# Kernel tuning notes

Measured on AMD Instinct MI355X. Metric: run time of the kernel, lower is better.

Reference implementation:

```python
import jax, jax.numpy as jnp
import numpy as np

DIM = 256
HEADS = 8
DIM_HEAD = 64
INNER = HEADS * DIM_HEAD  # 512
SCALE = DIM_HEAD ** -0.5
EPS = 1e-5


def _layernorm(x, w, b):
    mu = jnp.mean(x, axis=-1, keepdims=True)
    var = jnp.var(x, axis=-1, keepdims=True)
    return (x - mu) * jax.lax.rsqrt(var + EPS) * w + b


def setup_inputs() -> dict:
    key = jax.random.key(0)
    ks = jax.random.split(key, 20)
    B, N, M, H, W = 8, 4096, 256, 64, 64
    s = 0.02
    inp = {
        "feat": jax.random.normal(ks[0], (B, N, DIM), jnp.float32),
        "center": jax.random.normal(ks[1], (B, M, DIM), jnp.float32),
        "pos": jax.random.normal(ks[2], (B, DIM, H, W), jnp.float32),
        "center_pos": jax.random.normal(ks[3], (B, M, DIM), jnp.float32),
        # projection weights stored [in, out] so y = x @ W
        "Wq": jax.random.normal(ks[4], (DIM, INNER), jnp.float32) * s,
        "Wk": jax.random.normal(ks[5], (DIM, INNER), jnp.float32) * s,
        "Wv1": jax.random.normal(ks[6], (DIM, INNER), jnp.float32) * s,
        "Wv2": jax.random.normal(ks[7], (DIM, INNER), jnp.float32) * s,
        "Wo1": jax.random.normal(ks[8], (INNER, DIM), jnp.float32) * s,
        "Wo2": jax.random.normal(ks[9], (INNER, DIM), jnp.float32) * s,
        "ln1_w": jnp.ones((DIM,), jnp.float32),
        "ln1_b": jnp.zeros((DIM,), jnp.float32),
        "ln2_w": jnp.ones((DIM,), jnp.float32),
        "ln2_b": jnp.zeros((DIM,), jnp.float32),
        "ffn1_W1": jax.random.normal(ks[10], (DIM, DIM), jnp.float32) * s,
        "ffn1_W2": jax.random.normal(ks[11], (DIM, DIM), jnp.float32) * s,
        "ffn1_b2": jnp.zeros((DIM,), jnp.float32),
        "ffn2_W1": jax.random.normal(ks[12], (DIM, DIM), jnp.float32) * s,
        "ffn2_W2": jax.random.normal(ks[13], (DIM, DIM), jnp.float32) * s,
        "ffn2_b2": jnp.zeros((DIM,), jnp.float32),
    }
    return inp


def reference(feat, center, pos, center_pos, Wq, Wk, Wv1, Wv2, Wo1, Wo2,
              ln1_w, ln1_b, ln2_w, ln2_b, ffn1_W1, ffn1_W2, ffn1_b2,
              ffn2_W1, ffn2_W2, ffn2_b2):
    B = feat.shape[0]
    # pos: [B, C, H, W] -> [B, N, C]
    pos_f = pos.reshape(B, DIM, -1).transpose(0, 2, 1)
    q = (feat + pos_f) @ Wq            # [B, N, INNER]
    k = (center + center_pos) @ Wk     # [B, M, INNER]
    v1 = feat @ Wv1                    # [B, N, INNER]
    v2 = center @ Wv2                  # [B, M, INNER]

    def split(x):  # [B, T, h*d] -> [B, h, T, d]
        return x.reshape(B, x.shape[1], HEADS, DIM_HEAD).transpose(0, 2, 1, 3)

    q, k, v1, v2 = split(q), split(k), split(v1), split(v2)
    attn = jnp.einsum("bhnd,bhmd->bhnm", q, k) * SCALE  # [B, h, N, M]
    attn1 = jax.nn.softmax(attn, axis=-2)  # over N (queries)
    attn2 = jax.nn.softmax(attn, axis=-1)  # over M (keys)
    out_feat = jnp.einsum("bhnm,bhmd->bhnd", attn2, v2)    # [B, h, N, d]
    out_center = jnp.einsum("bhnm,bhnd->bhmd", attn1, v1)  # [B, h, M, d]

    def merge(x):  # [B, h, T, d] -> [B, T, h*d]
        return x.transpose(0, 2, 1, 3).reshape(B, x.shape[2], INNER)

    out_feat = merge(out_feat) @ Wo1 + feat
    out_center = merge(out_center) @ Wo2 + center
    out_feat = _layernorm(out_feat, ln1_w, ln1_b)
    out_center = _layernorm(out_center, ln2_w, ln2_b)
    out_feat = jax.nn.relu(out_feat @ ffn1_W1) @ ffn1_W2 + ffn1_b2 + out_feat
    out_center = jax.nn.relu(out_center @ ffn2_W1) @ ffn2_W2 + ffn2_b2 + out_center
    return out_feat, out_center
```

## Files before the change

### kernel.cpp

```cpp
#include <hip/hip_runtime.h>

typedef __bf16 bf16;
typedef __bf16 bf16x4 __attribute__((ext_vector_type(4)));
typedef __bf16 bf16x8 __attribute__((ext_vector_type(8)));
typedef float f32x4 __attribute__((ext_vector_type(4)));

#define MFMA16(a, b, c) __builtin_amdgcn_mfma_f32_16x16x32_bf16(a, b, c, 0, 0, 0)

#define CEXP 0.18033688011112042f

struct WTArgs {
  const float* src[10];
  bf16* dst[10];
  int K[10];
  int N[10];
};

__global__ __launch_bounds__(256) void wtrans_kernel(WTArgs args) {
  const int z = blockIdx.z;
  const int K = args.K[z], N = args.N[z];
  const int k0 = blockIdx.x * 64, n0 = blockIdx.y * 64;
  if (k0 >= K || n0 >= N) return;
  __shared__ float t[64][65];
  const int tx = threadIdx.x & 63, ty = threadIdx.x >> 6;
  const float* __restrict__ src = args.src[z];
  bf16* __restrict__ dst = args.dst[z];
#pragma unroll
  for (int i = 0; i < 16; ++i)
    t[ty + i * 4][tx] = src[(size_t)(k0 + ty + i * 4) * N + n0 + tx];
  __syncthreads();
#pragma unroll
  for (int i = 0; i < 16; ++i)
    dst[(size_t)(n0 + ty + i * 4) * K + k0 + tx] = (bf16)t[tx][ty + i * 4];
}

__global__ __launch_bounds__(256) void prep_xq_kernel(
    const float* __restrict__ feat, const float* __restrict__ pos,
    bf16* __restrict__ xq) {
  const int n0 = blockIdx.x * 64;
  const int c0 = blockIdx.y * 64;
  const int b = blockIdx.z;
  __shared__ float t[64][65];
  const int tx = threadIdx.x & 63, ty = threadIdx.x >> 6;
#pragma unroll
  for (int i = 0; i < 16; ++i) {
    int c = ty + i * 4;
    t[c][tx] = pos[((size_t)b * 256 + c0 + c) * 4096 + n0 + tx];
  }
  __syncthreads();
#pragma unroll
  for (int i = 0; i < 16; ++i) {
    int n = ty + i * 4;
    size_t off = ((size_t)b * 4096 + n0 + n) * 256 + c0 + tx;
    xq[off] = (bf16)(feat[off] + t[tx][n]);
  }
}

__global__ __launch_bounds__(256) void addvec_kernel(
    const float* __restrict__ a, const float* __restrict__ b,
    bf16* __restrict__ o, int n4) {
  int i = blockIdx.x * 256 + threadIdx.x;
  if (i < n4) {
    f32x4 x = ((const f32x4*)a)[i];
    f32x4 y = ((const f32x4*)b)[i];
    bf16x4 z;
#pragma unroll
    for (int j = 0; j < 4; ++j) z[j] = (bf16)(x[j] + y[j]);
    ((bf16x4*)o)[i] = z;
  }
}

template <typename TA>
__device__ inline bf16x8 ldA8(const TA* p);
template <>
__device__ inline bf16x8 ldA8<bf16>(const bf16* p) {
  return *(const bf16x8*)p;
}
template <>
__device__ inline bf16x8 ldA8<float>(const float* p) {
  f32x4 u = *(const f32x4*)p;
  f32x4 v = *((const f32x4*)p + 1);
  bf16x8 o;
#pragma unroll
  for (int i = 0; i < 4; ++i) {
    o[i] = (bf16)u[i];
    o[4 + i] = (bf16)v[i];
  }
  return o;
}

template <int EPI, typename TO, typename TR, typename TA>
__global__ __launch_bounds__(256) void gemm_kernel(
    const TA* __restrict__ A, const bf16* __restrict__ BT,
    TO* __restrict__ C, const TR* __restrict__ resid,
    const float* __restrict__ bias, int M, int N, int K) {
  const int m0 = blockIdx.x * 128;
  const int n0 = blockIdx.y * 128;
  const int tid = threadIdx.x;
  const int lane = tid & 63;
  const int w = tid >> 6;
  const int wr = (w >> 1) * 64, wc = (w & 1) * 64;
  const int l15 = lane & 15, quad = lane >> 4;

  __shared__ bf16 Al[128 * 40];
  __shared__ bf16 Bl[128 * 40];

  f32x4 acc[4][4];
#pragma unroll
  for (int i = 0; i < 4; ++i)
#pragma unroll
    for (int j = 0; j < 4; ++j) acc[i][j] = (f32x4){0.f, 0.f, 0.f, 0.f};

  for (int k0 = 0; k0 < K; k0 += 32) {
#pragma unroll
    for (int c = 0; c < 2; ++c) {
      int idx = tid + c * 256;
      int row = idx >> 2;
      int ko = (idx & 3) * 8;
      *(bf16x8*)(Al + row * 40 + ko) =
          ldA8(A + (size_t)(m0 + row) * K + k0 + ko);
      *(bf16x8*)(Bl + row * 40 + ko) =
          *(const bf16x8*)(BT + (size_t)(n0 + row) * K + k0 + ko);
    }
    __syncthreads();
    bf16x8 fa[4], fb[4];
#pragma unroll
    for (int i = 0; i < 4; ++i) {
      fa[i] = *(const bf16x8*)(Al + (wr + i * 16 + l15) * 40 + quad * 8);
      fb[i] = *(const bf16x8*)(Bl + (wc + i * 16 + l15) * 40 + quad * 8);
    }
#pragma unroll
    for (int i = 0; i < 4; ++i)
#pragma unroll
      for (int j = 0; j < 4; ++j)
        acc[i][j] = MFMA16(fa[i], fb[j], acc[i][j]);
    __syncthreads();
  }

#pragma unroll
  for (int i = 0; i < 4; ++i) {
#pragma unroll
    for (int r = 0; r < 4; ++r) {
      int row = m0 + wr + i * 16 + quad * 4 + r;
      size_t rb = (size_t)row * N + n0 + wc;
#pragma unroll
      for (int j = 0; j < 4; ++j) {
        int col = j * 16 + l15;
        float v = acc[i][j][r];
        if constexpr (EPI == 1) v = fmaxf(v, 0.f);
        if constexpr (EPI == 2) v += (float)resid[rb + col];
        if constexpr (EPI == 3)
          v += bias[n0 + wc + col] + (float)resid[rb + col];
        C[rb + col] = (TO)v;
      }
    }
  }
}

__global__ __launch_bounds__(256, 1) void attf_kernel(
    const bf16* q, const bf16* __restrict__ kk, const bf16* __restrict__ v1,
    const bf16* __restrict__ v2, bf16* af, float* __restrict__ acc_p,
    float* __restrict__ colsum_p) {
  const int nb = blockIdx.x;
  const int h = blockIdx.y;
  const int b = blockIdx.z;
  const int tid = threadIdx.x;
  const int lane = tid & 63;
  const int w = tid >> 6;
  const int l15 = lane & 15, quad = lane >> 4;

  __shared__ __align__(16) bf16 klds[256 * 72];
  __shared__ __align__(16) bf16 v2T[64 * 264];
  __shared__ __align__(16) bf16 v1T[2][64 * 72];
  __shared__ __align__(16) bf16 PT[256 * 72];
  __shared__ __align__(16) bf16 Pl[4][16 * 264];

#pragma unroll
  for (int c = 0; c < 8; ++c) {
    int idx = tid + c * 256;
    int m = idx >> 3;
    int dc = (idx & 7) * 8;
    *(bf16x8*)(klds + m * 72 + dc) =
        *(const bf16x8*)(kk + ((size_t)(b * 256 + m)) * 512 + h * 64 + dc);
  }
#pragma unroll
  for (int c = 0; c < 8; ++c) {
    int idx = tid + c * 256;
    int m = idx >> 3;
    int dc = (idx & 7) * 8;
    bf16x8 t =
        *(const bf16x8*)(v2 + ((size_t)(b * 256 + m)) * 512 + h * 64 + dc);
#pragma unroll
    for (int j = 0; j < 8; ++j) v2T[(dc + j) * 264 + m] = t[j];
  }
  {
    const int nl = tid >> 3;
    const int dc = (tid & 7) * 8;
    const bf16* v1b =
        v1 + ((size_t)(b * 4096 + nb * 1024)) * 512 + h * 64 + dc;
    bf16x8 t0 = *(const bf16x8*)(v1b + (size_t)nl * 512);
    bf16x8 t1 = *(const bf16x8*)(v1b + (size_t)(nl + 32) * 512);
#pragma unroll
    for (int j = 0; j < 8; ++j) {
      v1T[0][(dc + j) * 72 + nl] = t0[j];
      v1T[0][(dc + j) * 72 + nl + 32] = t1[j];
    }
  }
  bf16x8 qa0, qa1;
  {
    int nrow = b * 4096 + nb * 1024 + w * 16 + l15;
    const bf16* qp = q + (size_t)nrow * 512 + h * 64 + quad * 8;
    qa0 = *(const bf16x8*)(qp);
    qa1 = *(const bf16x8*)(qp + 32);
  }

  f32x4 oc2[16];
#pragma unroll
  for (int i = 0; i < 16; ++i) oc2[i] = (f32x4){0.f, 0.f, 0.f, 0.f};
  float cs[16];
#pragma unroll
  for (int i = 0; i < 16; ++i) cs[i] = 0.f;

  __syncthreads();

#pragma unroll 2
  for (int ch = 0; ch < 16; ++ch) {
    bf16x8 v1ra, v1rb;
    const int nl = tid >> 3;
    const int dc = (tid & 7) * 8;
    if (ch < 15) {
      const bf16* v1b =
          v1 + ((size_t)(b * 4096 + nb * 1024 + (ch + 1) * 64)) * 512 +
          h * 64 + dc;
      v1ra = *(const bf16x8*)(v1b + (size_t)nl * 512);
      v1rb = *(const bf16x8*)(v1b + (size_t)(nl + 32) * 512);
    }

    float rs[4] = {0.f, 0.f, 0.f, 0.f};
#pragma unroll
    for (int mt = 0; mt < 16; ++mt) {
      const bf16* kp = klds + (mt * 16 + l15) * 72 + quad * 8;
      bf16x8 b0 = *(const bf16x8*)(kp);
      bf16x8 b1 = *(const bf16x8*)(kp + 32);
      f32x4 s = (f32x4){0.f, 0.f, 0.f, 0.f};
      s = MFMA16(qa0, b0, s);
      s = MFMA16(qa1, b1, s);
      float e0 = exp2f(s[0] * CEXP);
      float e1 = exp2f(s[1] * CEXP);
      float e2 = exp2f(s[2] * CEXP);
      float e3 = exp2f(s[3] * CEXP);
      rs[0] += e0; rs[1] += e1; rs[2] += e2; rs[3] += e3;
      cs[mt] += e0 + e1 + e2 + e3;
      Pl[w][(quad * 4 + 0) * 264 + mt * 16 + l15] = (bf16)e0;
      Pl[w][(quad * 4 + 1) * 264 + mt * 16 + l15] = (bf16)e1;
      Pl[w][(quad * 4 + 2) * 264 + mt * 16 + l15] = (bf16)e2;
      Pl[w][(quad * 4 + 3) * 264 + mt * 16 + l15] = (bf16)e3;
      bf16x4 ev;
      ev[0] = (bf16)e0; ev[1] = (bf16)e1; ev[2] = (bf16)e2; ev[3] = (bf16)e3;
      *(bf16x4*)(PT + (mt * 16 + l15) * 72 + w * 16 + quad * 4) = ev;
    }
    if (ch < 15) {
      bf16* dst = v1T[(ch + 1) & 1];
#pragma unroll
      for (int j = 0; j < 8; ++j) {
        dst[(dc + j) * 72 + nl] = v1ra[j];
        dst[(dc + j) * 72 + nl + 32] = v1rb[j];
      }
    }
    __syncthreads();

    if (ch < 15) {
      int nrow = b * 4096 + nb * 1024 + (ch + 1) * 64 + w * 16 + l15;
      const bf16* qp = q + (size_t)nrow * 512 + h * 64 + quad * 8;
      qa0 = *(const bf16x8*)(qp);
      qa1 = *(const bf16x8*)(qp + 32);
    }

    f32x4 o1[4];
#pragma unroll
    for (int i = 0; i < 4; ++i) o1[i] = (f32x4){0.f, 0.f, 0.f, 0.f};
#pragma unroll
    for (int ks = 0; ks < 8; ++ks) {
      bf16x8 pa = *(const bf16x8*)(Pl[w] + l15 * 264 + ks * 32 + quad * 8);
#pragma unroll
      for (int dt = 0; dt < 4; ++dt) {
        bf16x8 vb = *(const bf16x8*)(v2T + (dt * 16 + l15) * 264 + ks * 32 +
                                     quad * 8);
        o1[dt] = MFMA16(pa, vb, o1[dt]);
      }
    }
    float inv[4];
#pragma unroll
    for (int r = 0; r < 4; ++r) {
      float v = rs[r];
      v += __shfl_xor(v, 1, 64);
      v += __shfl_xor(v, 2, 64);
      v += __shfl_xor(v, 4, 64);
      v += __shfl_xor(v, 8, 64);
      inv[r] = 1.f / v;
    }
#pragma unroll
    for (int dt = 0; dt < 4; ++dt) {
#pragma unroll
      for (int r = 0; r < 4; ++r) {
        int n = nb * 1024 + ch * 64 + w * 16 + quad * 4 + r;
        af[((size_t)(b * 4096 + n)) * 512 + h * 64 + dt * 16 + l15] =
            (bf16)(o1[dt][r] * inv[r]);
      }
    }

    const bf16* v1cur = v1T[ch & 1];
#pragma unroll
    for (int ks = 0; ks < 2; ++ks) {
      bf16x8 vb[4];
#pragma unroll
      for (int dt = 0; dt < 4; ++dt)
        vb[dt] = *(const bf16x8*)(v1cur + (dt * 16 + l15) * 72 + ks * 32 +
                                  quad * 8);
#pragma unroll
      for (int mq = 0; mq < 4; ++mq) {
        bf16x8 pa2 = *(const bf16x8*)(PT + (mq * 64 + w * 16 + l15) * 72 +
                                      ks * 32 + quad * 8);
#pragma unroll
        for (int dt = 0; dt < 4; ++dt)
          oc2[mq * 4 + dt] = MFMA16(pa2, vb[dt], oc2[mq * 4 + dt]);
      }
    }
    __syncthreads();
  }

  float* cw = (float*)klds;
#pragma unroll
  for (int t = 0; t < 16; ++t) {
    float v = cs[t];
    v += __shfl_xor(v, 16, 64);
    v += __shfl_xor(v, 32, 64);
    if (quad == 0) cw[w * 256 + t * 16 + l15] = v;
  }
  __syncthreads();
  {
    int m = tid;
    float s = cw[m] + cw[256 + m] + cw[512 + m] + cw[768 + m];
    colsum_p[((size_t)(nb * 64 + b * 8 + h)) * 256 + m] = s;
  }
  float* base = acc_p + ((size_t)(nb * 64 + b * 8 + h)) * 256 * 64;
#pragma unroll
  for (int mq = 0; mq < 4; ++mq) {
#pragma unroll
    for (int dt = 0; dt < 4; ++dt) {
#pragma unroll
      for (int r = 0; r < 4; ++r) {
        int m = mq * 64 + w * 16 + quad * 4 + r;
        base[m * 64 + dt * 16 + l15] = oc2[mq * 4 + dt][r];
      }
    }
  }
}

__global__ __launch_bounds__(256) void acm_kernel(
    const float* __restrict__ acc_p, const float* __restrict__ colsum_p,
    bf16* __restrict__ acm) {
  int idx = blockIdx.x * 256 + threadIdx.x;
  int d = idx & 63;
  int h = (idx >> 6) & 7;
  int m = (idx >> 9) & 255;
  int b = idx >> 17;
  float cv = 0.f, v = 0.f;
#pragma unroll
  for (int p = 0; p < 4; ++p) {
    cv += colsum_p[((size_t)(p * 64 + b * 8 + h)) * 256 + m];
    v += acc_p[(((size_t)(p * 64 + b * 8 + h)) * 256 + m) * 64 + d];
  }
  acm[idx] = (bf16)(v / cv);
}

__global__ __launch_bounds__(256) void ln_kernel(
    const bf16* __restrict__ x, const float* __restrict__ wv,
    const float* __restrict__ bv, bf16* __restrict__ y, int rows) {
  int wave = threadIdx.x >> 6;
  int lane = threadIdx.x & 63;
  int row = blockIdx.x * 4 + wave;
  if (row >= rows) return;
  const bf16* xr = x + (size_t)row * 256;
  bf16x4 v = *(const bf16x4*)(xr + lane * 4);
  float f0 = v[0], f1 = v[1], f2 = v[2], f3 = v[3];
  float s = f0 + f1 + f2 + f3;
  float ss = f0 * f0 + f1 * f1 + f2 * f2 + f3 * f3;
#pragma unroll
  for (int m = 1; m < 64; m <<= 1) {
    s += __shfl_xor(s, m, 64);
    ss += __shfl_xor(ss, m, 64);
  }
  float mean = s * (1.f / 256.f);
  float var = ss * (1.f / 256.f) - mean * mean;
  float rstd = rsqrtf(var + 1e-5f);
  f32x4 wq = *(const f32x4*)(wv + lane * 4);
  f32x4 bq = *(const f32x4*)(bv + lane * 4);
  bf16x4 o;
  o[0] = (bf16)((f0 - mean) * rstd * wq[0] + bq[0]);
  o[1] = (bf16)((f1 - mean) * rstd * wq[1] + bq[1]);
  o[2] = (bf16)((f2 - mean) * rstd * wq[2] + bq[2]);
  o[3] = (bf16)((f3 - mean) * rstd * wq[3] + bq[3]);
  *(bf16x4*)(y + (size_t)row * 256 + lane * 4) = o;
}

extern "C" void kernel_launch(void* const* d_in, const int* in_sizes, int n_in,
                              void* d_out, int out_size, void* d_ws,
                              size_t ws_size, hipStream_t stream) {
  const float* feat = (const float*)d_in[0];
  const float* center = (const float*)d_in[1];
  const float* pos = (const float*)d_in[2];
  const float* cpos = (const float*)d_in[3];
  const float* Wq = (const float*)d_in[4];
  const float* Wk = (const float*)d_in[5];
  const float* Wv1 = (const float*)d_in[6];
  const float* Wv2 = (const float*)d_in[7];
  const float* Wo1 = (const float*)d_in[8];
  const float* Wo2 = (const float*)d_in[9];
  const float* ln1w = (const float*)d_in[10];
  const float* ln1b = (const float*)d_in[11];
  const float* ln2w = (const float*)d_in[12];
  const float* ln2b = (const float*)d_in[13];
  const float* f1W1 = (const float*)d_in[14];
  const float* f1W2 = (const float*)d_in[15];
  const float* f1b2 = (const float*)d_in[16];
  const float* f2W1 = (const float*)d_in[17];
  const float* f2W2 = (const float*)d_in[18];
  const float* f2b2 = (const float*)d_in[19];

  char* ws = (char*)d_ws;
  const size_t MB = 1024 * 1024;
  bf16* q_ = (bf16*)(ws + 0);
  bf16* af_ = q_;
  bf16* v1_ = (bf16*)(ws + 32 * MB);
  bf16* xq_ = (bf16*)(ws + 64 * MB);
  float* accp_ = (float*)(ws + 64 * MB);
  bf16* rf_ = xq_;
  bf16* k_ = (bf16*)(ws + 80 * MB);
  bf16* xk_ = (bf16*)(ws + 82 * MB);
  bf16* rc_ = xk_;
  bf16* v2_ = (bf16*)(ws + 83 * MB);
  bf16* acm_ = v2_;
  float* colsum_ = (float*)(ws + 89 * MB);
  bf16* wt_ = (bf16*)(ws + 89 * MB + 262144);
  bf16* yf_ = q_;
  bf16* tf_ = (bf16*)(ws + 16 * MB);
  bf16* yc_ = (bf16*)(ws + 92 * MB);
  bf16* tc_ = (bf16*)(ws + 93 * MB);

  bf16* WqT = wt_;
  bf16* WkT = WqT + 131072;
  bf16* Wv1T = WkT + 131072;
  bf16* Wv2T = Wv1T + 131072;
  bf16* Wo1T = Wv2T + 131072;
  bf16* Wo2T = Wo1T + 131072;
  bf16* f1W1T = Wo2T + 131072;
  bf16* f1W2T = f1W1T + 65536;
  bf16* f2W1T = f1W2T + 65536;
  bf16* f2W2T = f2W1T + 65536;

  float* out_feat = (float*)d_out;
  float* out_center = out_feat + (size_t)8 * 4096 * 256;

  WTArgs wa;
  const float* srcs[10] = {Wq, Wk, Wv1, Wv2, Wo1, Wo2, f1W1, f1W2, f2W1, f2W2};
  bf16* dsts[10] = {WqT, WkT, Wv1T, Wv2T, Wo1T, Wo2T, f1W1T, f1W2T, f2W1T, f2W2T};
  int Ks[10] = {256, 256, 256, 256, 512, 512, 256, 256, 256, 256};
  int Ns[10] = {512, 512, 512, 512, 256, 256, 256, 256, 256, 256};
  for (int i = 0; i < 10; ++i) {
    wa.src[i] = srcs[i];
    wa.dst[i] = dsts[i];
    wa.K[i] = Ks[i];
    wa.N[i] = Ns[i];
  }

  wtrans_kernel<<<dim3(8, 8, 10), 256, 0, stream>>>(wa);
  prep_xq_kernel<<<dim3(64, 4, 8), 256, 0, stream>>>(feat, pos, xq_);
  addvec_kernel<<<dim3(512), 256, 0, stream>>>(center, cpos, xk_, 131072);

  gemm_kernel<0, bf16, bf16, bf16><<<dim3(256, 4), 256, 0, stream>>>(
      xq_, WqT, q_, nullptr, nullptr, 32768, 512, 256);
  gemm_kernel<0, bf16, bf16, bf16><<<dim3(16, 4), 256, 0, stream>>>(
      xk_, WkT, k_, nullptr, nullptr, 2048, 512, 256);
  gemm_kernel<0, bf16, bf16, float><<<dim3(256, 4), 256, 0, stream>>>(
      feat, Wv1T, v1_, nullptr, nullptr, 32768, 512, 256);
  gemm_kernel<0, bf16, bf16, float><<<dim3(16, 4), 256, 0, stream>>>(
      center, Wv2T, v2_, nullptr, nullptr, 2048, 512, 256);

  attf_kernel<<<dim3(4, 8, 8), 256, 0, stream>>>(q_, k_, v1_, v2_, af_, accp_,
                                                 colsum_);
  acm_kernel<<<dim3(4096), 256, 0, stream>>>(accp_, colsum_, acm_);

  gemm_kernel<2, bf16, float, bf16><<<dim3(256, 2), 256, 0, stream>>>(
      af_, Wo1T, rf_, feat, nullptr, 32768, 256, 512);
  ln_kernel<<<dim3(8192), 256, 0, stream>>>(rf_, ln1w, ln1b, yf_, 32768);
  gemm_kernel<1, bf16, bf16, bf16><<<dim3(256, 2), 256, 0, stream>>>(
      yf_, f1W1T, tf_, nullptr, nullptr, 32768, 256, 256);
  gemm_kernel<3, float, bf16, bf16><<<dim3(256, 2), 256, 0, stream>>>(
      tf_, f1W2T, out_feat, yf_, f1b2, 32768, 256, 256);

  gemm_kernel<2, bf16, float, bf16><<<dim3(16, 2), 256, 0, stream>>>(
      acm_, Wo2T, rc_, center, nullptr, 2048, 256, 512);
  ln_kernel<<<dim3(512), 256, 0, stream>>>(rc_, ln2w, ln2b, yc_, 2048);
  gemm_kernel<1, bf16, bf16, bf16><<<dim3(16, 2), 256, 0, stream>>>(
      yc_, f2W1T, tc_, nullptr, nullptr, 2048, 256, 256);
  gemm_kernel<3, float, bf16, bf16><<<dim3(16, 2), 256, 0, stream>>>(
      tc_, f2W2T, out_center, yc_, f2b2, 2048, 256, 256);
}
```

Measured before the change: 391.5 us.

## Restructure dual-softmax attention kernel with 512 threads, swizzled LDS, register-held P

Reworks the fused attention kernel to 8 waves per block and 128-row chunks. The k, v2, v1 and P tiles move from padded shared-memory layouts to XOR-swizzled ones. The S tile is computed transposed (K as the A operand), so each lane's P values can feed the P·V2 MFMA straight from registers, which removes the per-wave Pl buffer. Column sums are now computed with an MFMA against a ones vector instead of shuffle reductions through shared memory. These changes target LDS bank conflicts, shared-memory traffic and VGPR pressure, while the larger block and __launch_bounds__(512, 2) add wave-level parallelism; the more complex index math and the bf16-rounded column sums are the cost.

```diff
diff --git a/kernel.cpp b/kernel.cpp
--- a/kernel.cpp
+++ b/kernel.cpp
@@ -157,7 +157,7 @@
   }
 }
 
-__global__ __launch_bounds__(256, 1) void attf_kernel(
+__global__ __launch_bounds__(512, 2) void attf_kernel(
     const bf16* q, const bf16* __restrict__ kk, const bf16* __restrict__ v1,
     const bf16* __restrict__ v2, bf16* af, float* __restrict__ acc_p,
     float* __restrict__ colsum_p) {
@@ -169,41 +169,44 @@
   const int w = tid >> 6;
   const int l15 = lane & 15, quad = lane >> 4;
 
-  __shared__ __align__(16) bf16 klds[256 * 72];
-  __shared__ __align__(16) bf16 v2T[64 * 264];
-  __shared__ __align__(16) bf16 v1T[2][64 * 72];
-  __shared__ __align__(16) bf16 PT[256 * 72];
-  __shared__ __align__(16) bf16 Pl[4][16 * 264];
-
-#pragma unroll
-  for (int c = 0; c < 8; ++c) {
-    int idx = tid + c * 256;
-    int m = idx >> 3;
-    int dc = (idx & 7) * 8;
-    *(bf16x8*)(klds + m * 72 + dc) =
+  __shared__ __align__(16) bf16 klds[256 * 64];
+  __shared__ __align__(16) bf16 v2T[64 * 256];
+  __shared__ __align__(16) bf16 v1T[2][64 * 128];
+  __shared__ __align__(16) bf16 PS[256 * 128];
+
+#pragma unroll
+  for (int c = 0; c < 4; ++c) {
+    int idx = tid + c * 512;
+    int m = idx >> 3, dc = (idx & 7) * 8;
+    bf16x8 t =
         *(const bf16x8*)(kk + ((size_t)(b * 256 + m)) * 512 + h * 64 + dc);
-  }
-#pragma unroll
-  for (int c = 0; c < 8; ++c) {
-    int idx = tid + c * 256;
-    int m = idx >> 3;
-    int dc = (idx & 7) * 8;
+    *(bf16x8*)(klds + ((m * 64 + dc) ^ ((m & 7) << 3))) = t;
+  }
+#pragma unroll
+  for (int c = 0; c < 4; ++c) {
+    int idx = tid + c * 512;
+    int m = idx & 255, dc = (idx >> 8) * 8;
     bf16x8 t =
         *(const bf16x8*)(v2 + ((size_t)(b * 256 + m)) * 512 + h * 64 + dc);
-#pragma unroll
-    for (int j = 0; j < 8; ++j) v2T[(dc + j) * 264 + m] = t[j];
+    int p = (m & ~31) |
+            (((((m >> 2) & 3) << 3) + (m & 3)) + (((m >> 4) & 1) << 2));
+#pragma unroll
+    for (int j = 0; j < 8; ++j) {
+      int d = dc + j;
+      v2T[(d * 256 + p) ^ ((d & 7) << 3)] = t[j];
+    }
   }
   {
-    const int nl = tid >> 3;
-    const int dc = (tid & 7) * 8;
-    const bf16* v1b =
-        v1 + ((size_t)(b * 4096 + nb * 1024)) * 512 + h * 64 + dc;
-    bf16x8 t0 = *(const bf16x8*)(v1b + (size_t)nl * 512);
-    bf16x8 t1 = *(const bf16x8*)(v1b + (size_t)(nl + 32) * 512);
+    int n = tid & 127, dg = tid >> 7;
+    const bf16* vp =
+        v1 + ((size_t)(b * 4096 + nb * 1024 + n)) * 512 + h * 64 + dg * 8;
+    bf16x8 t0 = *(const bf16x8*)(vp);
+    bf16x8 t1 = *(const bf16x8*)(vp + 32);
 #pragma unroll
     for (int j = 0; j < 8; ++j) {
-      v1T[0][(dc + j) * 72 + nl] = t0[j];
-      v1T[0][(dc + j) * 72 + nl + 32] = t1[j];
+      int d0 = dg * 8 + j, d1 = d0 + 32;
+      v1T[0][(d0 * 128 + n) ^ ((d0 & 7) << 3)] = t0[j];
+      v1T[0][(d1 * 128 + n) ^ ((d1 & 7) << 3)] = t1[j];
     }
   }
   bf16x8 qa0, qa1;
@@ -214,147 +217,147 @@
     qa1 = *(const bf16x8*)(qp + 32);
   }
 
-  f32x4 oc2[16];
-#pragma unroll
-  for (int i = 0; i < 16; ++i) oc2[i] = (f32x4){0.f, 0.f, 0.f, 0.f};
-  float cs[16];
-#pragma unroll
-  for (int i = 0; i < 16; ++i) cs[i] = 0.f;
+  f32x4 oc2[8];
+#pragma unroll
+  for (int i = 0; i < 8; ++i) oc2[i] = (f32x4){0.f, 0.f, 0.f, 0.f};
+  f32x4 csa[2];
+  csa[0] = (f32x4){0.f, 0.f, 0.f, 0.f};
+  csa[1] = (f32x4){0.f, 0.f, 0.f, 0.f};
+  bf16x8 ones8;
+#pragma unroll
+  for (int j = 0; j < 8; ++j) ones8[j] = (bf16)1.0f;
+  const int nloc = w * 16 + l15;
 
   __syncthreads();
 
-#pragma unroll 2
-  for (int ch = 0; ch < 16; ++ch) {
-    bf16x8 v1ra, v1rb;
-    const int nl = tid >> 3;
-    const int dc = (tid & 7) * 8;
-    if (ch < 15) {
-      const bf16* v1b =
-          v1 + ((size_t)(b * 4096 + nb * 1024 + (ch + 1) * 64)) * 512 +
-          h * 64 + dc;
-      v1ra = *(const bf16x8*)(v1b + (size_t)nl * 512);
-      v1rb = *(const bf16x8*)(v1b + (size_t)(nl + 32) * 512);
-    }
-
-    float rs[4] = {0.f, 0.f, 0.f, 0.f};
+  for (int ch = 0; ch < 8; ++ch) {
+    bf16x8 v1a, v1b;
+    const int vn = tid & 127, vdg = tid >> 7;
+    if (ch < 7) {
+      const bf16* vp =
+          v1 + ((size_t)(b * 4096 + nb * 1024 + (ch + 1) * 128 + vn)) * 512 +
+          h * 64 + vdg * 8;
+      v1a = *(const bf16x8*)(vp);
+      v1b = *(const bf16x8*)(vp + 32);
+    }
+
+    bf16x8 pa[8];
+    float rs = 0.f;
 #pragma unroll
     for (int mt = 0; mt < 16; ++mt) {
-      const bf16* kp = klds + (mt * 16 + l15) * 72 + quad * 8;
-      bf16x8 b0 = *(const bf16x8*)(kp);
-      bf16x8 b1 = *(const bf16x8*)(kp + 32);
+      int mrow = mt * 16 + l15;
+      int kb = mrow * 64;
+      int sw = (mrow & 7) << 3;
+      bf16x8 ka = *(const bf16x8*)(klds + ((kb + quad * 8) ^ sw));
+      bf16x8 kc = *(const bf16x8*)(klds + ((kb + 32 + quad * 8) ^ sw));
       f32x4 s = (f32x4){0.f, 0.f, 0.f, 0.f};
-      s = MFMA16(qa0, b0, s);
-      s = MFMA16(qa1, b1, s);
+      s = MFMA16(ka, qa0, s);
+      s = MFMA16(kc, qa1, s);
       float e0 = exp2f(s[0] * CEXP);
       float e1 = exp2f(s[1] * CEXP);
       float e2 = exp2f(s[2] * CEXP);
       float e3 = exp2f(s[3] * CEXP);
-      rs[0] += e0; rs[1] += e1; rs[2] += e2; rs[3] += e3;
-      cs[mt] += e0 + e1 + e2 + e3;
-      Pl[w][(quad * 4 + 0) * 264 + mt * 16 + l15] = (bf16)e0;
-      Pl[w][(quad * 4 + 1) * 264 + mt * 16 + l15] = (bf16)e1;
-      Pl[w][(quad * 4 + 2) * 264 + mt * 16 + l15] = (bf16)e2;
-      Pl[w][(quad * 4 + 3) * 264 + mt * 16 + l15] = (bf16)e3;
-      bf16x4 ev;
-      ev[0] = (bf16)e0; ev[1] = (bf16)e1; ev[2] = (bf16)e2; ev[3] = (bf16)e3;
-      *(bf16x4*)(PT + (mt * 16 + l15) * 72 + w * 16 + quad * 4) = ev;
-    }
-    if (ch < 15) {
+      rs += (e0 + e1) + (e2 + e3);
+      bf16 b0 = (bf16)e0, b1 = (bf16)e1, b2 = (bf16)e2, b3 = (bf16)e3;
+      int m0 = mt * 16 + quad * 4;
+      PS[((m0 + 0) * 128 + nloc) ^ (((m0 + 0) & 7) << 3)] = b0;
+      PS[((m0 + 1) * 128 + nloc) ^ (((m0 + 1) & 7) << 3)] = b1;
+      PS[((m0 + 2) * 128 + nloc) ^ (((m0 + 2) & 7) << 3)] = b2;
+      PS[((m0 + 3) * 128 + nloc) ^ (((m0 + 3) & 7) << 3)] = b3;
+      pa[mt >> 1][(mt & 1) * 4 + 0] = b0;
+      pa[mt >> 1][(mt & 1) * 4 + 1] = b1;
+      pa[mt >> 1][(mt & 1) * 4 + 2] = b2;
+      pa[mt >> 1][(mt & 1) * 4 + 3] = b3;
+    }
+
+    f32x4 o1[4];
+#pragma unroll
+    for (int i = 0; i < 4; ++i) o1[i] = (f32x4){0.f, 0.f, 0.f, 0.f};
+#pragma unroll
+    for (int ks = 0; ks < 8; ++ks) {
+#pragma unroll
+      for (int dt = 0; dt < 4; ++dt) {
+        int d = dt * 16 + l15;
+        bf16x8 vb = *(const bf16x8*)(v2T +
+                                     ((d * 256 + ks * 32 + quad * 8) ^
+                                      ((d & 7) << 3)));
+        o1[dt] = MFMA16(pa[ks], vb, o1[dt]);
+      }
+    }
+
+    float rsf = rs + __shfl_xor(rs, 16, 64);
+    rsf += __shfl_xor(rsf, 32, 64);
+#pragma unroll
+    for (int r = 0; r < 4; ++r) {
+      float iv = 1.f / __shfl(rsf, (lane & 48) | (quad * 4 + r), 64);
+      int n = nb * 1024 + ch * 128 + w * 16 + quad * 4 + r;
+      bf16* ap = af + ((size_t)(b * 4096 + n)) * 512 + h * 64 + l15;
+#pragma unroll
+      for (int dt = 0; dt < 4; ++dt)
+        ap[dt * 16] = (bf16)(o1[dt][r] * iv);
+    }
+
+    if (ch < 7) {
       bf16* dst = v1T[(ch + 1) & 1];
 #pragma unroll
       for (int j = 0; j < 8; ++j) {
-        dst[(dc + j) * 72 + nl] = v1ra[j];
-        dst[(dc + j) * 72 + nl + 32] = v1rb[j];
+        int d0 = vdg * 8 + j, d1 = d0 + 32;
+        dst[(d0 * 128 + vn) ^ ((d0 & 7) << 3)] = v1a[j];
+        dst[(d1 * 128 + vn) ^ ((d1 & 7) << 3)] = v1b[j];
       }
     }
     __syncthreads();
 
-    if (ch < 15) {
-      int nrow = b * 4096 + nb * 1024 + (ch + 1) * 64 + w * 16 + l15;
+    bf16x8 qn0 = qa0, qn1 = qa1;
+    if (ch < 7) {
+      int nrow = b * 4096 + nb * 1024 + (ch + 1) * 128 + w * 16 + l15;
       const bf16* qp = q + (size_t)nrow * 512 + h * 64 + quad * 8;
-      qa0 = *(const bf16x8*)(qp);
-      qa1 = *(const bf16x8*)(qp + 32);
-    }
-
-    f32x4 o1[4];
-#pragma unroll
-    for (int i = 0; i < 4; ++i) o1[i] = (f32x4){0.f, 0.f, 0.f, 0.f};
-#pragma unroll
-    for (int ks = 0; ks < 8; ++ks) {
-      bf16x8 pa = *(const bf16x8*)(Pl[w] + l15 * 264 + ks * 32 + quad * 8);
+      qn0 = *(const bf16x8*)(qp);
+      qn1 = *(const bf16x8*)(qp + 32);
+    }
+    const bf16* vc = v1T[ch & 1];
+#pragma unroll
+    for (int ks = 0; ks < 4; ++ks) {
+      bf16x8 vbv[4];
 #pragma unroll
       for (int dt = 0; dt < 4; ++dt) {
-        bf16x8 vb = *(const bf16x8*)(v2T + (dt * 16 + l15) * 264 + ks * 32 +
-                                     quad * 8);
-        o1[dt] = MFMA16(pa, vb, o1[dt]);
+        int d = dt * 16 + l15;
+        vbv[dt] = *(const bf16x8*)(vc + ((d * 128 + ks * 32 + quad * 8) ^
+                                         ((d & 7) << 3)));
       }
-    }
-    float inv[4];
-#pragma unroll
-    for (int r = 0; r < 4; ++r) {
-      float v = rs[r];
-      v += __shfl_xor(v, 1, 64);
-      v += __shfl_xor(v, 2, 64);
-      v += __shfl_xor(v, 4, 64);
-      v += __shfl_xor(v, 8, 64);
-      inv[r] = 1.f / v;
-    }
-#pragma unroll
-    for (int dt = 0; dt < 4; ++dt) {
-#pragma unroll
-      for (int r = 0; r < 4; ++r) {
-        int n = nb * 1024 + ch * 64 + w * 16 + quad * 4 + r;
-        af[((size_t)(b * 4096 + n)) * 512 + h * 64 + dt * 16 + l15] =
-            (bf16)(o1[dt][r] * inv[r]);
+#pragma unroll
+      for (int mr = 0; mr < 2; ++mr) {
+        int m = w * 32 + mr * 16 + l15;
+        bf16x8 pa2 = *(const bf16x8*)(PS + ((m * 128 + ks * 32 + quad * 8) ^
+                                            ((m & 7) << 3)));
+#pragma unroll
+        for (int dt = 0; dt < 4; ++dt)
+          oc2[mr * 4 + dt] = MFMA16(pa2, vbv[dt], oc2[mr * 4 + dt]);
+        csa[mr] = MFMA16(pa2, ones8, csa[mr]);
       }
     }
-
-    const bf16* v1cur = v1T[ch & 1];
-#pragma unroll
-    for (int ks = 0; ks < 2; ++ks) {
-      bf16x8 vb[4];
-#pragma unroll
-      for (int dt = 0; dt < 4; ++dt)
-        vb[dt] = *(const bf16x8*)(v1cur + (dt * 16 + l15) * 72 + ks * 32 +
-                                  quad * 8);
-#pragma unroll
-      for (int mq = 0; mq < 4; ++mq) {
-        bf16x8 pa2 = *(const bf16x8*)(PT + (mq * 64 + w * 16 + l15) * 72 +
-                                      ks * 32 + quad * 8);
-#pragma unroll
-        for (int dt = 0; dt < 4; ++dt)
-          oc2[mq * 4 + dt] = MFMA16(pa2, vb[dt], oc2[mq * 4 + dt]);
-      }
-    }
     __syncthreads();
-  }
-
-  float* cw = (float*)klds;
-#pragma unroll
-  for (int t = 0; t < 16; ++t) {
-    float v = cs[t];
-    v += __shfl_xor(v, 16, 64);
-    v += __shfl_xor(v, 32, 64);
-    if (quad == 0) cw[w * 256 + t * 16 + l15] = v;
-  }
-  __syncthreads();
-  {
-    int m = tid;
-    float s = cw[m] + cw[256 + m] + cw[512 + m] + cw[768 + m];
-    colsum_p[((size_t)(nb * 64 + b * 8 + h)) * 256 + m] = s;
-  }
-  float* base = acc_p + ((size_t)(nb * 64 + b * 8 + h)) * 256 * 64;
-#pragma unroll
-  for (int mq = 0; mq < 4; ++mq) {
-#pragma unroll
-    for (int dt = 0; dt < 4; ++dt) {
-#pragma unroll
-      for (int r = 0; r < 4; ++r) {
-        int m = mq * 64 + w * 16 + quad * 4 + r;
-        base[m * 64 + dt * 16 + l15] = oc2[mq * 4 + dt][r];
-      }
-    }
-  }
+    qa0 = qn0;
+    qa1 = qn1;
+  }
+
+  const size_t slab = (size_t)(nb * 64 + b * 8 + h);
+  if (l15 == 0) {
+#pragma unroll
+    for (int mr = 0; mr < 2; ++mr)
+#pragma unroll
+      for (int r = 0; r < 4; ++r)
+        colsum_p[slab * 256 + w * 32 + mr * 16 + quad * 4 + r] = csa[mr][r];
+  }
+  float* base = acc_p + slab * (256 * 64);
+#pragma unroll
+  for (int mr = 0; mr < 2; ++mr)
+#pragma unroll
+    for (int dt = 0; dt < 4; ++dt)
+#pragma unroll
+      for (int r = 0; r < 4; ++r)
+        base[(w * 32 + mr * 16 + quad * 4 + r) * 64 + dt * 16 + l15] =
+            oc2[mr * 4 + dt][r];
 }
 
 __global__ __launch_bounds__(256) void acm_kernel(
@@ -487,7 +490,7 @@
   gemm_kernel<0, bf16, bf16, float><<<dim3(16, 4), 256, 0, stream>>>(
       center, Wv2T, v2_, nullptr, nullptr, 2048, 512, 256);
 
-  attf_kernel<<<dim3(4, 8, 8), 256, 0, stream>>>(q_, k_, v1_, v2_, af_, accp_,
+  attf_kernel<<<dim3(4, 8, 8), 512, 0, stream>>>(q_, k_, v1_, v2_, af_, accp_,
                                                  colsum_);
   acm_kernel<<<dim3(4096), 256, 0, stream>>>(accp_, colsum_, acm_);
 
```

Result: slower. 443.3 us (+13.2%).
